# Optimization experiments

Hardware: AMD Instinct MI355X
Metric: run time of the kernel (lower is better)

Reference implementation:

```python
import jax, jax.numpy as jnp
import numpy as np

B, C, H, W = 8, 64, 64, 64
CQ = C // 8  # query/key channels


def setup_inputs() -> dict:
    key = jax.random.key(0)
    ks = jax.random.split(key, 7)
    s = 0.05
    return {
        "x": jax.random.normal(ks[0], (B, C, H, W), jnp.float32),
        "wq": jax.random.normal(ks[1], (CQ, C), jnp.float32) * s,
        "bq": jnp.zeros((CQ,), jnp.float32),
        "wk": jax.random.normal(ks[2], (CQ, C), jnp.float32) * s,
        "bk": jnp.zeros((CQ,), jnp.float32),
        "wv": jax.random.normal(ks[3], (C, C), jnp.float32) * s,
        "bv": jnp.zeros((C,), jnp.float32),
    }


def reference(x, wq, bq, wk, bk, wv, bv):
    b, c, h, w = x.shape
    n = h * w
    xf = x.reshape(b, c, n)                       # [B, C, N]
    # 1x1 convs == per-pixel linear over channels
    q = jnp.einsum('oc,bcn->bon', wq, xf) + bq[None, :, None]   # [B, CQ, N]
    k = jnp.einsum('oc,bcn->bon', wk, xf) + bk[None, :, None]   # [B, CQ, N]
    v = jnp.einsum('oc,bcn->bon', wv, xf) + bv[None, :, None]   # [B, C, N]
    # energy[b, i, j] = q[b, :, i] . k[b, :, j]  (unscaled)
    energy = jnp.einsum('bci,bcj->bij', q, k)     # [B, N, N]
    attention = jax.nn.softmax(energy, axis=-1)   # softmax over j
    # out[b, c, i] = sum_j v[b, c, j] * attention[b, i, j]
    out = jnp.einsum('bcj,bij->bci', v, attention)
    return out.reshape(b, c, h, w)
```

## Files before the change

### kernel.cpp

```cpp
#include <hip/hip_runtime.h>
#include <hip/hip_bf16.h>


#define B_   8
#define C_   64
#define N_   4096
#define LOG2E 1.44269504088896340736f

typedef short bf16x8 __attribute__((ext_vector_type(8)));
typedef float f32x4  __attribute__((ext_vector_type(4)));
typedef unsigned int uint32;

#if __has_builtin(__builtin_amdgcn_exp2f)
#define EXP2(x) __builtin_amdgcn_exp2f(x)
#else
#define EXP2(x) __expf((x) * 0.69314718055994530942f)
#endif

__device__ __forceinline__ unsigned short f2bf_rn(float f) {
    union { __hip_bfloat16 h; unsigned short u; } cv;
    cv.h = __float2bfloat16(f);
    return cv.u;
}
__device__ __forceinline__ uint32 pk_rn(float lo, float hi) {
    return (uint32)f2bf_rn(lo) | ((uint32)f2bf_rn(hi) << 16);
}
__device__ __forceinline__ uint32 pack_rtz(float lo, float hi) {
    return __builtin_amdgcn_perm(__float_as_uint(hi), __float_as_uint(lo), 0x07060302);
}

__global__ __launch_bounds__(256) void prep_kernel(
    const float* __restrict__ x,
    const float* __restrict__ wq, const float* __restrict__ bq,
    const float* __restrict__ wk, const float* __restrict__ bk,
    unsigned short* __restrict__ Qh, unsigned short* __restrict__ Kh,
    unsigned short* __restrict__ Xb)
{
    __shared__ float Xs[C_][64];
    __shared__ float Wqk[16][C_];
    __shared__ float Bqk[16];

    const int t  = threadIdx.x;
    const int b  = blockIdx.x >> 6;
    const int p0 = (blockIdx.x & 63) << 6;

    #pragma unroll
    for (int k = 0; k < 4; ++k) {
        int i = t + k * 256;
        int o = i >> 6;
        Wqk[o][i & 63] = (o < 8) ? wq[i] * LOG2E : wk[i - 512];
    }
    if (t < 16) Bqk[t] = (t < 8) ? bq[t] * LOG2E : bk[t - 8];

    #pragma unroll
    for (int k = 0; k < 4; ++k) {
        int i = t + k * 256;
        int c = i >> 4, p4 = (i & 15) << 2;
        const float4 v = *(const float4*)(x + ((size_t)b * C_ + c) * N_ + p0 + p4);
        *(float4*)&Xs[c][p4] = v;
        uint2 u;
        u.x = pk_rn(v.x, v.y);
        u.y = pk_rn(v.z, v.w);
        *(uint2*)(Xb + ((size_t)b * C_ + c) * N_ + p0 + p4) = u;
    }
    __syncthreads();

    const int pix = t & 63, grp = t >> 6;
    float a[4];
    #pragma unroll
    for (int r = 0; r < 4; ++r) a[r] = Bqk[grp * 4 + r];
    #pragma unroll
    for (int c = 0; c < C_; ++c) {
        float xv = Xs[c][pix];
        #pragma unroll
        for (int r = 0; r < 4; ++r) a[r] += Wqk[grp * 4 + r][c] * xv;
    }
    uint2 u;
    u.x = pk_rn(a[0], a[1]);
    u.y = pk_rn(a[2], a[3]);
    unsigned short* dst = (grp & 2) ? Kh : Qh;
    *(uint2*)(dst + ((size_t)b * N_ + p0 + pix) * 8 + (grp & 1) * 4) = u;
}

__global__ __launch_bounds__(512, 4) void attn_mfma9_kernel(
    const unsigned short* __restrict__ Qh,
    const unsigned short* __restrict__ Kh,
    const unsigned short* __restrict__ Xb,
    const float* __restrict__ wv, const float* __restrict__ bv,
    float* __restrict__ out)
{
    __shared__ __align__(16) char smem[67584];

    const int t    = threadIdx.x;
    const int w    = t >> 6;
    const int lane = t & 63;
    const int l16  = lane & 15;
    const int qd   = lane >> 4;
    const int p    = w & 3;
    const int h    = w >> 2;
    const int b    = blockIdx.x >> 6;
    const int i0   = (blockIdx.x & 63) << 6;

    const bf16x8 z8 = {};
    const f32x4  zf = {};

    bf16x8 qf[4];
    #pragma unroll
    for (int qt = 0; qt < 4; ++qt) {
        qf[qt] = z8;
        if (qd == 0)
            qf[qt] = *(const bf16x8*)(Qh + ((size_t)b * N_ + i0 + qt * 16 + l16) * 8);
    }

    const unsigned short* Kp = Kh + ((size_t)b * N_ + p * 1024 + h * 16) * 8;
    const unsigned short* Xp = Xb + ((size_t)b * C_ + h * 32) * N_ + p * 1024;

    f32x4 acc[2][4];
    #pragma unroll
    for (int ct = 0; ct < 2; ++ct)
        #pragma unroll
        for (int qt = 0; qt < 4; ++qt) acc[ct][qt] = zf;
    float dsum[4] = {0.f, 0.f, 0.f, 0.f};

    const int swz   = (l16 & 3) << 2;
    const int pbase = p * 8192 + l16 * 64;
    const int woff  = ((h * 8 + qd * 2) ^ swz) << 2;
    const int roff  = ((qd * 4) ^ swz) << 2;

    bf16x8 kf[2], xf[2][2];
    kf[0] = z8;
    if (qd == 0) kf[0] = *(const bf16x8*)(Kp + (size_t)l16 * 8);
    #pragma unroll
    for (int ct = 0; ct < 2; ++ct)
        xf[0][ct] = *(const bf16x8*)(Xp + (size_t)(ct * 16 + l16) * N_ + qd * 8);

    #pragma unroll 2
    for (int s = 0; s < 32; ++s) {
        const int cur = s & 1, nxt = cur ^ 1;
        const int jb = s * 32;
        char* pb_ = smem + pbase + cur * 4096;

        f32x4 sf[4];
        #pragma unroll
        for (int qt = 0; qt < 4; ++qt)
            sf[qt] = __builtin_amdgcn_mfma_f32_16x16x32_bf16(kf[cur], qf[qt], zf, 0, 0, 0);

        if (s < 31) {
            bf16x8 nk = z8;
            if (qd == 0) nk = *(const bf16x8*)(Kp + (size_t)(jb + 32 + l16) * 8);
            kf[nxt] = nk;
            #pragma unroll
            for (int ct = 0; ct < 2; ++ct)
                xf[nxt][ct] = *(const bf16x8*)(Xp + (size_t)(ct * 16 + l16) * N_ + jb + 32 + qd * 8);
        }

        #pragma unroll
        for (int qt = 0; qt < 4; ++qt) {
            float e0 = EXP2(sf[qt][0]);
            float e1 = EXP2(sf[qt][1]);
            float e2 = EXP2(sf[qt][2]);
            float e3 = EXP2(sf[qt][3]);
            dsum[qt] += (e0 + e1) + (e2 + e3);
            uint2 u;
            u.x = pack_rtz(e0, e1);
            u.y = pack_rtz(e2, e3);
            *(uint2*)(pb_ + qt * 1024 + woff) = u;
        }

        __syncthreads();

        #pragma unroll
        for (int qt = 0; qt < 4; ++qt) {
            bf16x8 pbf = *(const bf16x8*)(pb_ + qt * 1024 + roff);
            #pragma unroll
            for (int ct = 0; ct < 2; ++ct)
                acc[ct][qt] = __builtin_amdgcn_mfma_f32_16x16x32_bf16(xf[cur][ct], pbf, acc[ct][qt], 0, 0, 0);
        }
    }

    #pragma unroll
    for (int qt = 0; qt < 4; ++qt) {
        float v = dsum[qt];
        v += __shfl_xor(v, 16, 64);
        v += __shfl_xor(v, 32, 64);
        if (qd == 0) *(float*)(smem + 65536 + (w * 64 + qt * 16 + l16) * 4) = v;
    }

    __syncthreads();
    if (p != 0) {
        const int slot = h * 3 + (p - 1);
        char* rb = smem + slot * 8192;
        #pragma unroll
        for (int ct = 0; ct < 2; ++ct)
            #pragma unroll
            for (int qt = 0; qt < 4; ++qt)
                *(f32x4*)(rb + (ct * 4 + qt) * 1024 + lane * 16) = acc[ct][qt];
    }
    __syncthreads();
    if (p == 0) {
        #pragma unroll
        for (int rr = 0; rr < 3; ++rr) {
            const char* rb = smem + (h * 3 + rr) * 8192;
            #pragma unroll
            for (int ct = 0; ct < 2; ++ct)
                #pragma unroll
                for (int qt = 0; qt < 4; ++qt)
                    acc[ct][qt] += *(const f32x4*)(rb + (ct * 4 + qt) * 1024 + lane * 16);
        }
        float* Or = (float*)(smem + 49152);
        #pragma unroll
        for (int ct = 0; ct < 2; ++ct)
            #pragma unroll
            for (int qt = 0; qt < 4; ++qt)
                #pragma unroll
                for (int r = 0; r < 4; ++r)
                    Or[(h * 32 + ct * 16 + qd * 4 + r) * 64 + qt * 16 + l16] = acc[ct][qt][r];
    }
    __syncthreads();
    {
        float* Wvs = (float*)smem;
        for (int i = t; i < 4096; i += 512) Wvs[i] = wv[i];
    }
    __syncthreads();

    const int q = t & 63, grp = t >> 6;
    const float* Wvs = (const float*)smem;
    const float* Or  = (const float*)(smem + 49152);
    const float* Dn  = (const float*)(smem + 65536);
    float dtot = 0.f;
    #pragma unroll
    for (int r = 0; r < 8; ++r) dtot += Dn[r * 64 + q];
    const float inv = 1.0f / dtot;
    float o[8];
    #pragma unroll
    for (int r = 0; r < 8; ++r) o[r] = 0.f;
    for (int k = 0; k < 64; ++k) {
        float ov = Or[k * 64 + q];
        #pragma unroll
        for (int r = 0; r < 8; ++r)
            o[r] += Wvs[(grp * 8 + r) * 64 + k] * ov;
    }
    #pragma unroll
    for (int r = 0; r < 8; ++r)
        out[((size_t)b * C_ + grp * 8 + r) * N_ + i0 + q] = o[r] * inv + bv[grp * 8 + r];
}

__global__ __launch_bounds__(256) void attn_fused_fallback(
    const float* __restrict__ x,
    const float* __restrict__ wq, const float* __restrict__ bq,
    const float* __restrict__ wk, const float* __restrict__ bk,
    const float* __restrict__ wv, const float* __restrict__ bv,
    float* __restrict__ out)
{
    __shared__ float Qs[64][8];
    __shared__ float Ks[8][64];
    __shared__ float Vs[64][C_];
    __shared__ float Ws[64][64 + 1];
    __shared__ float Xs[C_ * 64];
    __shared__ float Wks[8][C_];
    __shared__ float Wvs[C_][C_ + 1];

    const int t     = threadIdx.x;
    const int b     = blockIdx.x / (N_ / 64);
    const int i0    = (blockIdx.x % (N_ / 64)) * 64;
    const int jlane = t & 63;
    const int wgrp  = t >> 6;

    for (int l = t; l < 8 * C_;  l += 256) Wks[l >> 6][l & 63] = wk[l];
    for (int l = t; l < C_ * C_; l += 256) Wvs[l >> 6][l & 63] = wv[l];
    for (int l = t; l < C_ * 64; l += 256)
        Xs[(l >> 6) * 64 + (l & 63)] = x[((size_t)b * C_ + (l >> 6)) * N_ + i0 + (l & 63)];
    __syncthreads();
    {
        int qi = jlane;
        #pragma unroll
        for (int r = 0; r < 2; ++r) {
            int cc = wgrp * 2 + r;
            float a = bq[cc];
            for (int c = 0; c < C_; ++c) a += wq[cc * C_ + c] * Xs[c * 64 + qi];
            Qs[qi][cc] = a;
        }
    }
    __syncthreads();

    const int qi2 = t >> 2;
    const int cb  = (t & 3) << 4;
    float accv[16];
    #pragma unroll
    for (int r = 0; r < 16; ++r) accv[r] = 0.f;
    float denom = 0.f;

    for (int j0 = 0; j0 < N_; j0 += 64) {
        for (int l = t; l < C_ * 64; l += 256)
            Xs[(l >> 6) * 64 + (l & 63)] = x[((size_t)b * C_ + (l >> 6)) * N_ + j0 + (l & 63)];
        __syncthreads();
        {
            int j = jlane;
            #pragma unroll
            for (int r = 0; r < 2; ++r) {
                int cc = wgrp * 2 + r;
                float a = bk[cc];
                for (int c = 0; c < C_; ++c) a += Wks[cc][c] * Xs[c * 64 + j];
                Ks[cc][j] = a;
            }
        }
        {
            int vc = jlane;
            #pragma unroll 2
            for (int r = 0; r < 16; ++r) {
                int j = wgrp * 16 + r;
                float a = bv[vc];
                for (int c = 0; c < C_; ++c) a += Wvs[vc][c] * Xs[c * 64 + j];
                Vs[j][vc] = a;
            }
        }
        __syncthreads();
        {
            float kreg[8];
            #pragma unroll
            for (int cc = 0; cc < 8; ++cc) kreg[cc] = Ks[cc][jlane];
            #pragma unroll 4
            for (int r = 0; r < 16; ++r) {
                int qi = wgrp * 16 + r;
                float e = 0.f;
                #pragma unroll
                for (int cc = 0; cc < 8; ++cc) e += Qs[qi][cc] * kreg[cc];
                Ws[qi][jlane] = __expf(e);
            }
        }
        __syncthreads();
        #pragma unroll 4
        for (int j = 0; j < 64; ++j) {
            float wv2 = Ws[qi2][j];
            denom += wv2;
            const float4* vrow = (const float4*)(&Vs[j][cb]);
            float4 v0 = vrow[0], v1 = vrow[1], v2 = vrow[2], v3 = vrow[3];
            accv[0]  += wv2 * v0.x; accv[1]  += wv2 * v0.y; accv[2]  += wv2 * v0.z; accv[3]  += wv2 * v0.w;
            accv[4]  += wv2 * v1.x; accv[5]  += wv2 * v1.y; accv[6]  += wv2 * v1.z; accv[7]  += wv2 * v1.w;
            accv[8]  += wv2 * v2.x; accv[9]  += wv2 * v2.y; accv[10] += wv2 * v2.z; accv[11] += wv2 * v2.w;
            accv[12] += wv2 * v3.x; accv[13] += wv2 * v3.y; accv[14] += wv2 * v3.z; accv[15] += wv2 * v3.w;
        }
        __syncthreads();
    }

    const float inv = 1.0f / denom;
    #pragma unroll
    for (int r = 0; r < 16; ++r)
        out[((size_t)b * C_ + cb + r) * N_ + i0 + qi2] = accv[r] * inv;
}

extern "C" void kernel_launch(void* const* d_in, const int* in_sizes, int n_in,
                              void* d_out, int out_size, void* d_ws, size_t ws_size,
                              hipStream_t stream)
{
    const float* x  = (const float*)d_in[0];
    const float* wq = (const float*)d_in[1];
    const float* bq = (const float*)d_in[2];
    const float* wk = (const float*)d_in[3];
    const float* bk = (const float*)d_in[4];
    const float* wv = (const float*)d_in[5];
    const float* bv = (const float*)d_in[6];
    float* out = (float*)d_out;

    const size_t nQ = (size_t)B_ * N_ * 8;
    const size_t nX = (size_t)B_ * C_ * N_;
    const size_t needed = (2 * nQ + nX) * sizeof(unsigned short);

    if (ws_size >= needed) {
        unsigned short* Qh = (unsigned short*)d_ws;
        unsigned short* Kh = Qh + nQ;
        unsigned short* Xb = Kh + nQ;
        prep_kernel<<<B_ * (N_ / 64), 256, 0, stream>>>(x, wq, bq, wk, bk, Qh, Kh, Xb);
        attn_mfma9_kernel<<<B_ * (N_ / 64), 512, 0, stream>>>(Qh, Kh, Xb, wv, bv, out);
    } else {
        attn_fused_fallback<<<B_ * (N_ / 64), 256, 0, stream>>>(x, wq, bq, wk, bk, wv, bv, out);
    }
}
```

Before: 118.9 us.

## Process two key sub-tiles per barrier to halve block synchronisations

The attention main loop now handles 64 keys per iteration instead of 32. It computes and exponentiates two 32-key score tiles into a doubled per-wave LDS probability buffer, then issues one __syncthreads before both PV MFMA passes. The goal is to halve barrier count and give the scheduler more independent MFMA/exp work between syncs. In exchange it uses more LDS for the probability buffers, adds register pressure, and changes the K/X prefetch pattern: X fragments are now reloaded right after use rather than a full step ahead.

```diff
diff --git a/kernel.cpp b/kernel.cpp
--- a/kernel.cpp
+++ b/kernel.cpp
@@ -82,7 +82,7 @@
     *(uint2*)(dst + ((size_t)b * N_ + p0 + pix) * 8 + (grp & 1) * 4) = u;
 }
 
-__global__ __launch_bounds__(512, 4) void attn_mfma9_kernel(
+__global__ __launch_bounds__(512, 4) void attn_mfma11_kernel(
     const unsigned short* __restrict__ Qh,
     const unsigned short* __restrict__ Kh,
     const unsigned short* __restrict__ Xb,
@@ -123,48 +123,74 @@
     float dsum[4] = {0.f, 0.f, 0.f, 0.f};
 
     const int swz   = (l16 & 3) << 2;
-    const int pbase = p * 8192 + l16 * 64;
+    const int pbase = p * 16384 + l16 * 64;
     const int woff  = ((h * 8 + qd * 2) ^ swz) << 2;
     const int roff  = ((qd * 4) ^ swz) << 2;
 
     bf16x8 kf[2], xf[2][2];
-    kf[0] = z8;
-    if (qd == 0) kf[0] = *(const bf16x8*)(Kp + (size_t)l16 * 8);
-    #pragma unroll
-    for (int ct = 0; ct < 2; ++ct)
-        xf[0][ct] = *(const bf16x8*)(Xp + (size_t)(ct * 16 + l16) * N_ + qd * 8);
+    kf[0] = z8; kf[1] = z8;
+    if (qd == 0) {
+        kf[0] = *(const bf16x8*)(Kp + (size_t)l16 * 8);
+        kf[1] = *(const bf16x8*)(Kp + (size_t)(32 + l16) * 8);
+    }
+    #pragma unroll
+    for (int u = 0; u < 2; ++u)
+        #pragma unroll
+        for (int ct = 0; ct < 2; ++ct)
+            xf[u][ct] = *(const bf16x8*)(Xp + (size_t)(ct * 16 + l16) * N_ + u * 32 + qd * 8);
 
     #pragma unroll 2
-    for (int s = 0; s < 32; ++s) {
-        const int cur = s & 1, nxt = cur ^ 1;
-        const int jb = s * 32;
-        char* pb_ = smem + pbase + cur * 4096;
-
-        f32x4 sf[4];
-        #pragma unroll
-        for (int qt = 0; qt < 4; ++qt)
-            sf[qt] = __builtin_amdgcn_mfma_f32_16x16x32_bf16(kf[cur], qf[qt], zf, 0, 0, 0);
-
-        if (s < 31) {
-            bf16x8 nk = z8;
-            if (qd == 0) nk = *(const bf16x8*)(Kp + (size_t)(jb + 32 + l16) * 8);
-            kf[nxt] = nk;
-            #pragma unroll
-            for (int ct = 0; ct < 2; ++ct)
-                xf[nxt][ct] = *(const bf16x8*)(Xp + (size_t)(ct * 16 + l16) * N_ + jb + 32 + qd * 8);
-        }
-
-        #pragma unroll
-        for (int qt = 0; qt < 4; ++qt) {
-            float e0 = EXP2(sf[qt][0]);
-            float e1 = EXP2(sf[qt][1]);
-            float e2 = EXP2(sf[qt][2]);
-            float e3 = EXP2(sf[qt][3]);
-            dsum[qt] += (e0 + e1) + (e2 + e3);
-            uint2 u;
-            u.x = pack_rtz(e0, e1);
-            u.y = pack_rtz(e2, e3);
-            *(uint2*)(pb_ + qt * 1024 + woff) = u;
+    for (int it = 0; it < 16; ++it) {
+        const int cur = it & 1;
+        const int jb = it * 64;
+        char* pb_ = smem + pbase + cur * 8192;
+
+        {
+            f32x4 sf[4];
+            #pragma unroll
+            for (int qt = 0; qt < 4; ++qt)
+                sf[qt] = __builtin_amdgcn_mfma_f32_16x16x32_bf16(kf[0], qf[qt], zf, 0, 0, 0);
+            #pragma unroll
+            for (int qt = 0; qt < 4; ++qt) {
+                float e0 = EXP2(sf[qt][0]);
+                float e1 = EXP2(sf[qt][1]);
+                float e2 = EXP2(sf[qt][2]);
+                float e3 = EXP2(sf[qt][3]);
+                dsum[qt] += (e0 + e1) + (e2 + e3);
+                uint2 u;
+                u.x = pack_rtz(e0, e1);
+                u.y = pack_rtz(e2, e3);
+                *(uint2*)(pb_ + qt * 1024 + woff) = u;
+            }
+        }
+        {
+            f32x4 sf[4];
+            #pragma unroll
+            for (int qt = 0; qt < 4; ++qt)
+                sf[qt] = __builtin_amdgcn_mfma_f32_16x16x32_bf16(kf[1], qf[qt], zf, 0, 0, 0);
+
+            if (it < 15) {
+                bf16x8 nk0 = z8, nk1 = z8;
+                if (qd == 0) {
+                    nk0 = *(const bf16x8*)(Kp + (size_t)(jb + 64 + l16) * 8);
+                    nk1 = *(const bf16x8*)(Kp + (size_t)(jb + 96 + l16) * 8);
+                }
+                kf[0] = nk0;
+                kf[1] = nk1;
+            }
+
+            #pragma unroll
+            for (int qt = 0; qt < 4; ++qt) {
+                float e0 = EXP2(sf[qt][0]);
+                float e1 = EXP2(sf[qt][1]);
+                float e2 = EXP2(sf[qt][2]);
+                float e3 = EXP2(sf[qt][3]);
+                dsum[qt] += (e0 + e1) + (e2 + e3);
+                uint2 u;
+                u.x = pack_rtz(e0, e1);
+                u.y = pack_rtz(e2, e3);
+                *(uint2*)(pb_ + 4096 + qt * 1024 + woff) = u;
+            }
         }
 
         __syncthreads();
@@ -174,7 +200,24 @@
             bf16x8 pbf = *(const bf16x8*)(pb_ + qt * 1024 + roff);
             #pragma unroll
             for (int ct = 0; ct < 2; ++ct)
-                acc[ct][qt] = __builtin_amdgcn_mfma_f32_16x16x32_bf16(xf[cur][ct], pbf, acc[ct][qt], 0, 0, 0);
+                acc[ct][qt] = __builtin_amdgcn_mfma_f32_16x16x32_bf16(xf[0][ct], pbf, acc[ct][qt], 0, 0, 0);
+        }
+        if (it < 15) {
+            #pragma unroll
+            for (int ct = 0; ct < 2; ++ct)
+                xf[0][ct] = *(const bf16x8*)(Xp + (size_t)(ct * 16 + l16) * N_ + jb + 64 + qd * 8);
+        }
+        #pragma unroll
+        for (int qt = 0; qt < 4; ++qt) {
+            bf16x8 pbf = *(const bf16x8*)(pb_ + 4096 + qt * 1024 + roff);
+            #pragma unroll
+            for (int ct = 0; ct < 2; ++ct)
+                acc[ct][qt] = __builtin_amdgcn_mfma_f32_16x16x32_bf16(xf[1][ct], pbf, acc[ct][qt], 0, 0, 0);
+        }
+        if (it < 15) {
+            #pragma unroll
+            for (int ct = 0; ct < 2; ++ct)
+                xf[1][ct] = *(const bf16x8*)(Xp + (size_t)(ct * 16 + l16) * N_ + jb + 96 + qd * 8);
         }
     }
 
@@ -371,7 +414,7 @@
         unsigned short* Kh = Qh + nQ;
         unsigned short* Xb = Kh + nQ;
         prep_kernel<<<B_ * (N_ / 64), 256, 0, stream>>>(x, wq, bq, wk, bk, Qh, Kh, Xb);
-        attn_mfma9_kernel<<<B_ * (N_ / 64), 512, 0, stream>>>(Qh, Kh, Xb, wv, bv, out);
+        attn_mfma11_kernel<<<B_ * (N_ / 64), 512, 0, stream>>>(Qh, Kh, Xb, wv, bv, out);
     } else {
         attn_fused_fallback<<<B_ * (N_ / 64), 256, 0, stream>>>(x, wq, bq, wk, bk, wv, bv, out);
     }
```

Result: slower. 205.3 us (+72.8%).
